# Performance work log

Measured on AMD Instinct MI355X. Metric: run time of the kernel, lower is better.

Reference implementation:

```python
import jax, jax.numpy as jnp
import numpy as np

B, S, D, H = 64, 512, 512, 512


def setup_inputs() -> dict:
    key = jax.random.key(0)
    ks = jax.random.split(key, 8)
    k = 1.0 / np.sqrt(H)  # torch nn.LSTM init bound
    return {
        "x": jax.random.normal(ks[0], (B, S, D), dtype=jnp.float32),
        "emb": jax.random.normal(ks[1], (B, D), dtype=jnp.float32),
        "h_n": jax.random.normal(ks[2], (1, B, H), dtype=jnp.float32),
        "c_n": jax.random.normal(ks[3], (1, B, H), dtype=jnp.float32),
        "W_ih": jax.random.uniform(ks[4], (4 * H, D), jnp.float32, -k, k),
        "W_hh": jax.random.uniform(ks[5], (4 * H, H), jnp.float32, -k, k),
        "b_ih": jax.random.uniform(ks[6], (4 * H,), jnp.float32, -k, k),
        "b_hh": jax.random.uniform(ks[7], (4 * H,), jnp.float32, -k, k),
    }


def reference(x, emb, h_n, c_n, W_ih, W_hh, b_ih, b_hh):
    # Decoder feeds emb at step 0, then teacher-forces x[:, i-1] at step i.
    inputs = jnp.concatenate([emb[:, None, :], x[:, :-1, :]], axis=1)  # [B,S,D]
    # Precompute input-to-hidden gates for the whole sequence (one big GEMM).
    xg = jnp.einsum("bsd,gd->bsg", inputs, W_ih) + b_ih + b_hh  # [B,S,4H]

    def step(carry, xg_t):
        h, c = carry
        gates = xg_t + h @ W_hh.T  # [B,4H]; torch gate order: i,f,g,o
        i, f, g, o = jnp.split(gates, 4, axis=-1)
        c = jax.nn.sigmoid(f) * c + jax.nn.sigmoid(i) * jnp.tanh(g)
        h = jax.nn.sigmoid(o) * jnp.tanh(c)
        return (h, c), h

    (_, _), ys = jax.lax.scan(step, (h_n[0], c_n[0]), jnp.swapaxes(xg, 0, 1))
    return jnp.swapaxes(ys, 0, 1)  # [B,S,H]
```

## Files before the change

### kernel.cpp

```cpp
#include <hip/hip_runtime.h>
#include <cstdint>


#define SS 512
#define DD 512
#define HH 512

typedef __attribute__((ext_vector_type(8))) short s8;
typedef __attribute__((ext_vector_type(4))) float f4;

__device__ inline short f2bf(float f) {
  unsigned u = __float_as_uint(f);
  u += 0x7fffu + ((u >> 16) & 1u);
  return (short)(u >> 16);
}

__device__ inline s8 cvt8(f4 a, f4 b) {
  s8 v;
  v[0]=f2bf(a[0]); v[1]=f2bf(a[1]); v[2]=f2bf(a[2]); v[3]=f2bf(a[3]);
  v[4]=f2bf(b[0]); v[5]=f2bf(b[1]); v[6]=f2bf(b[2]); v[7]=f2bf(b[3]);
  return v;
}

__device__ inline float sigm(float x)  { return 1.f / (1.f + __expf(-x)); }
__device__ inline float tanh_f(float x){ return 1.f - 2.f / (__expf(2.f*x) + 1.f); }

__device__ inline void stq_agent(void* p, unsigned long long v) {
  __hip_atomic_store((unsigned long long*)p, v, __ATOMIC_RELAXED, __HIP_MEMORY_SCOPE_AGENT);
}
__device__ inline unsigned long long ldq_agent(const void* p) {
  return __hip_atomic_load((const unsigned long long*)p, __ATOMIC_RELAXED, __HIP_MEMORY_SCOPE_AGENT);
}
__device__ inline void st4_agent(unsigned* p, unsigned v) {
  __hip_atomic_store(p, v, __ATOMIC_RELAXED, __HIP_MEMORY_SCOPE_AGENT);
}
__device__ inline unsigned ld4_agent(const unsigned* p) {
  return __hip_atomic_load(p, __ATOMIC_RELAXED, __HIP_MEMORY_SCOPE_AGENT);
}
__device__ inline void drain_vm() {
  asm volatile("s_waitcnt vmcnt(0)" ::: "memory");
}

__device__ inline void heavy_barrier(unsigned* cnt, unsigned target) {
  drain_vm();
  __syncthreads();
  if (threadIdx.x == 0) {
    __threadfence();
    __hip_atomic_fetch_add(cnt, 1u, __ATOMIC_RELAXED, __HIP_MEMORY_SCOPE_AGENT);
    unsigned guard = 0;
    while (__hip_atomic_load(cnt, __ATOMIC_RELAXED, __HIP_MEMORY_SCOPE_AGENT) < target) {
      __builtin_amdgcn_s_sleep(2);
      if (++guard > 10000000u) break;
    }
  }
  __syncthreads();
  (void)__hip_atomic_load(cnt, __ATOMIC_ACQUIRE, __HIP_MEMORY_SCOPE_AGENT);
  __syncthreads();
}

__launch_bounds__(256, 1)
__global__ void lstm_kernel(const float* __restrict__ x,   const float* __restrict__ emb,
                            const float* __restrict__ h_n, const float* __restrict__ c_n,
                            const float* __restrict__ W_ih, const float* __restrict__ W_hh,
                            const float* __restrict__ b_ih, const float* __restrict__ b_hh,
                            float* __restrict__ out, char* __restrict__ ws)
{
  const int tid  = threadIdx.x;
  const int wave = tid >> 6, lane = tid & 63;
  const int quad = lane >> 4, n = lane & 15;
  const int c  = blockIdx.x & 7;
  const int wg = blockIdx.x >> 3;

  unsigned* cnt   = (unsigned*)(ws + (size_t)c * 128);
  unsigned* flags = (unsigned*)(ws + 1024 + (size_t)c * 128);
  char*     hbuf  = ws + 4096;
  char*     xfrag = ws + 4096 + 2*8*8192;
  char*     xfc   = xfrag + (size_t)c * ((size_t)SS * 8192);

  __shared__ float lout[2][128];

  {
    int widc = wg*4 + wave;
    for (int item = widc; item < 4096; item += 128) {
      int t = item & 511, bl = item >> 9;
      const float* src = (t == 0) ? (emb + (size_t)(c*8 + bl) * DD)
                                  : (x + ((size_t)(c*8 + bl) * SS + (t-1)) * DD);
      f4 f0 = *(const f4*)(src + lane*8);
      f4 f1 = *(const f4*)(src + lane*8 + 4);
      s8 v = cvt8(f0, f1);
      *(s8*)(xfc + (size_t)t*8192 + (lane>>2)*512 + (lane&3)*128 + bl*16) = v;
    }
  }

  s8 wihf[16], whhf[16];
  {
    int r = wave*16 + n;
    int rowg = (r & 3)*512 + wg*16 + (r >> 2);
    const float* pih = W_ih + (size_t)rowg * DD + quad*8;
    const float* phh = W_hh + (size_t)rowg * HH + quad*8;
#pragma unroll
    for (int kk = 0; kk < 16; ++kk) {
      f4 a0 = *(const f4*)(pih + kk*32);
      f4 a1 = *(const f4*)(pih + kk*32 + 4);
      wihf[kk] = cvt8(a0, a1);
      f4 b0 = *(const f4*)(phh + kk*32);
      f4 b1 = *(const f4*)(phh + kk*32 + 4);
      whhf[kk] = cvt8(b0, b1);
    }
  }

  const int u = wg*16 + wave*4 + quad;
  f4 biasv;
  biasv[0] = b_ih[0*512+u] + b_hh[0*512+u];
  biasv[1] = b_ih[1*512+u] + b_hh[1*512+u];
  biasv[2] = b_ih[2*512+u] + b_hh[2*512+u];
  biasv[3] = b_ih[3*512+u] + b_hh[3*512+u];
  float creg = 0.f, h0 = 0.f;
  if (n < 8) {
    creg = c_n[(size_t)(c*8 + n)*HH + u];
    h0   = h_n[(size_t)(c*8 + n)*HH + u];
  }
  const int u0 = wg*16 + wave*4;
  const int hsoff = (u0>>5)*512 + ((u0>>3)&3)*128 + (u0&7)*2;

  {
    int sv = (int)(unsigned short)f2bf(h0);
    int p2 = sv | (__shfl_xor(sv, 16) << 16);
    int p4 = __shfl_xor(p2, 32);
    unsigned long long packed = (unsigned)p2 | ((unsigned long long)(unsigned)p4 << 32);
    if (lane < 8) stq_agent(hbuf + (size_t)c*8192 + hsoff + lane*16, packed);
  }

  heavy_barrier(cnt, 32u);

  const s8 zero8 = {0,0,0,0,0,0,0,0};
  s8 xf[16], hf[16];
#pragma unroll
  for (int kk = 0; kk < 16; ++kk) { xf[kk] = zero8; hf[kk] = zero8; }

  f4 accx = biasv, accx2 = {0.f,0.f,0.f,0.f};
  if (n < 8) {
    const char* xb = xfc + quad*128 + n*16;
#pragma unroll
    for (int kk = 0; kk < 16; ++kk)
      xf[kk] = *(const s8*)(xb + kk*512);
  }
#pragma unroll
  for (int kk = 0; kk < 8; ++kk)
    accx  = __builtin_amdgcn_mfma_f32_16x16x32_bf16(wihf[kk],   xf[kk],   accx,  0,0,0);
#pragma unroll
  for (int kk = 0; kk < 8; ++kk)
    accx2 = __builtin_amdgcn_mfma_f32_16x16x32_bf16(wihf[kk+8], xf[kk+8], accx2, 0,0,0);

  float* const outb = out + (size_t)(c*8)*SS*HH + wg*16;

  for (int t = 0; t < SS; ++t) {
    if (t > 0) {
      if (tid < 64) {
        const unsigned* fp = flags + (lane & 31);
        unsigned guard = 0; bool ok;
        do {
          ok = (ld4_agent(fp) >= (unsigned)t);
          if (++guard > 100000u) break;
        } while (!__all(ok));
      }
      __syncthreads();
    }

    const char* hrd = hbuf + (size_t)(((t  )&1)*8 + c)*8192;
    char*       hwr = hbuf + (size_t)(((t+1)&1)*8 + c)*8192;

    if (n < 8) {
      const char* b0 = hrd + quad*128 + n*16;
      union { unsigned long long qq[2]; s8 v; } tmp;
#pragma unroll
      for (int kk = 0; kk < 16; ++kk) {
        tmp.qq[0] = ldq_agent(b0 + kk*512);
        tmp.qq[1] = ldq_agent(b0 + kk*512 + 8);
        hf[kk] = tmp.v;
      }
    }

    f4 acc = accx, acc2 = accx2;
#pragma unroll
    for (int kk = 0; kk < 8; ++kk)
      acc  = __builtin_amdgcn_mfma_f32_16x16x32_bf16(whhf[kk],   hf[kk],   acc,  0,0,0);
#pragma unroll
    for (int kk = 0; kk < 8; ++kk)
      acc2 = __builtin_amdgcn_mfma_f32_16x16x32_bf16(whhf[kk+8], hf[kk+8], acc2, 0,0,0);
    acc += acc2;

    float iv = sigm(acc[0]);
    float fv = sigm(acc[1]);
    float gv = tanh_f(acc[2]);
    float ov = sigm(acc[3]);
    creg = fv*creg + iv*gv;
    float hv = ov * tanh_f(creg);

    if (n < 8) lout[t&1][n*16 + wave*4 + quad] = hv;

    if (t < SS-1) {
      int sv = (int)(unsigned short)f2bf(hv);
      int p2 = sv | (__shfl_xor(sv, 16) << 16);
      int p4 = __shfl_xor(p2, 32);
      unsigned long long packed = (unsigned)p2 | ((unsigned long long)(unsigned)p4 << 32);
      if (lane < 8) stq_agent(hwr + hsoff + lane*16, packed);
    }

    drain_vm();
    __syncthreads();

    if (t < SS-1 && tid == 0)
      st4_agent(flags + wg, (unsigned)(t + 1));

    if (tid < 128) {
      int n2 = tid >> 4, ul = tid & 15;
      outb[((size_t)n2*SS + t)*HH + ul] = lout[t&1][n2*16 + ul];
    }

    if (t < SS-1) {
      if (n < 8) {
        const char* xb = xfc + (size_t)(t+1)*8192 + quad*128 + n*16;
#pragma unroll
        for (int kk = 0; kk < 16; ++kk)
          xf[kk] = *(const s8*)(xb + kk*512);
      }
      accx = biasv; accx2[0]=0.f; accx2[1]=0.f; accx2[2]=0.f; accx2[3]=0.f;
#pragma unroll
      for (int kk = 0; kk < 8; ++kk)
        accx  = __builtin_amdgcn_mfma_f32_16x16x32_bf16(wihf[kk],   xf[kk],   accx,  0,0,0);
#pragma unroll
      for (int kk = 0; kk < 8; ++kk)
        accx2 = __builtin_amdgcn_mfma_f32_16x16x32_bf16(wihf[kk+8], xf[kk+8], accx2, 0,0,0);
    }
  }
}

extern "C" void kernel_launch(void* const* d_in, const int* in_sizes, int n_in,
                              void* d_out, int out_size, void* d_ws, size_t ws_size,
                              hipStream_t stream) {
  const float* x    = (const float*)d_in[0];
  const float* emb  = (const float*)d_in[1];
  const float* h_n  = (const float*)d_in[2];
  const float* c_n  = (const float*)d_in[3];
  const float* W_ih = (const float*)d_in[4];
  const float* W_hh = (const float*)d_in[5];
  const float* b_ih = (const float*)d_in[6];
  const float* b_hh = (const float*)d_in[7];

  hipMemsetAsync(d_ws, 0, 2048, stream);

  lstm_kernel<<<dim3(256), dim3(256), 0, stream>>>(
      x, emb, h_n, c_n, W_ih, W_hh, b_ih, b_hh, (float*)d_out, (char*)d_ws);
}
```

Before: 1.672 ms.

## Replace block-wide step barrier with per-wave flag counters and partial h prefetch

```diff
diff --git a/kernel.cpp b/kernel.cpp
--- a/kernel.cpp
+++ b/kernel.cpp
@@ -31,14 +31,17 @@
 __device__ inline unsigned long long ldq_agent(const void* p) {
   return __hip_atomic_load((const unsigned long long*)p, __ATOMIC_RELAXED, __HIP_MEMORY_SCOPE_AGENT);
 }
-__device__ inline void st4_agent(unsigned* p, unsigned v) {
-  __hip_atomic_store(p, v, __ATOMIC_RELAXED, __HIP_MEMORY_SCOPE_AGENT);
-}
 __device__ inline unsigned ld4_agent(const unsigned* p) {
   return __hip_atomic_load(p, __ATOMIC_RELAXED, __HIP_MEMORY_SCOPE_AGENT);
 }
 __device__ inline void drain_vm() {
   asm volatile("s_waitcnt vmcnt(0)" ::: "memory");
+}
+
+__device__ inline unsigned flag_ballot(const unsigned* flags, int lane, unsigned target) {
+  unsigned v = ld4_agent(flags + (lane & 31));
+  unsigned long long b = __ballot(v >= target);
+  return (unsigned)b & (unsigned)(b >> 32);
 }
 
 __device__ inline void heavy_barrier(unsigned* cnt, unsigned target) {
@@ -85,8 +88,8 @@
       int t = item & 511, bl = item >> 9;
       const float* src = (t == 0) ? (emb + (size_t)(c*8 + bl) * DD)
                                   : (x + ((size_t)(c*8 + bl) * SS + (t-1)) * DD);
-      f4 f0 = *(const f4*)(src + lane*8);
-      f4 f1 = *(const f4*)(src + lane*8 + 4);
+      f4 f0 = __builtin_nontemporal_load((const f4*)(src + lane*8));
+      f4 f1 = __builtin_nontemporal_load((const f4*)(src + lane*8 + 4));
       s8 v = cvt8(f0, f1);
       *(s8*)(xfc + (size_t)t*8192 + (lane>>2)*512 + (lane&3)*128 + bl*16) = v;
     }
@@ -143,7 +146,7 @@
     const char* xb = xfc + quad*128 + n*16;
 #pragma unroll
     for (int kk = 0; kk < 16; ++kk)
-      xf[kk] = *(const s8*)(xb + kk*512);
+      xf[kk] = __builtin_nontemporal_load((const s8*)(xb + kk*512));
   }
 #pragma unroll
   for (int kk = 0; kk < 8; ++kk)
@@ -152,32 +155,45 @@
   for (int kk = 0; kk < 8; ++kk)
     accx2 = __builtin_amdgcn_mfma_f32_16x16x32_bf16(wihf[kk+8], xf[kk+8], accx2, 0,0,0);
 
+  unsigned pm = 0xFFFFu;
+  unsigned rdy = 0u;
+  if (n < 8) {
+    const char* b0 = hbuf + (size_t)c*8192 + quad*128 + n*16;
+#pragma unroll
+    for (int kk = 0; kk < 16; ++kk) {
+      union { unsigned long long qq[2]; s8 v; } tmp;
+      tmp.qq[0] = ldq_agent(b0 + kk*512);
+      tmp.qq[1] = ldq_agent(b0 + kk*512 + 8);
+      hf[kk] = tmp.v;
+    }
+  }
+
   float* const outb = out + (size_t)(c*8)*SS*HH + wg*16;
 
   for (int t = 0; t < SS; ++t) {
-    if (t > 0) {
-      if (tid < 64) {
-        const unsigned* fp = flags + (lane & 31);
-        unsigned guard = 0; bool ok;
-        do {
-          ok = (ld4_agent(fp) >= (unsigned)t);
-          if (++guard > 100000u) break;
-        } while (!__all(ok));
-      }
-      __syncthreads();
-    }
-
     const char* hrd = hbuf + (size_t)(((t  )&1)*8 + c)*8192;
     char*       hwr = hbuf + (size_t)(((t+1)&1)*8 + c)*8192;
-
-    if (n < 8) {
-      const char* b0 = hrd + quad*128 + n*16;
-      union { unsigned long long qq[2]; s8 v; } tmp;
+    const unsigned tgt = 4u * (unsigned)t;
+
+    if (pm != 0xFFFFu) {
 #pragma unroll
       for (int kk = 0; kk < 16; ++kk) {
-        tmp.qq[0] = ldq_agent(b0 + kk*512);
-        tmp.qq[1] = ldq_agent(b0 + kk*512 + 8);
-        hf[kk] = tmp.v;
+        if (!(pm & (1u << kk))) {
+          const unsigned need = 3u << (2*kk);
+          unsigned guard = 0;
+          while ((rdy & need) != need) {
+            rdy |= flag_ballot(flags, lane, tgt);
+            asm volatile("" ::: "memory");
+            if (++guard > 1000000u) break;
+          }
+          if (n < 8) {
+            const char* b0 = hrd + quad*128 + n*16;
+            union { unsigned long long qq[2]; s8 v; } tmp;
+            tmp.qq[0] = ldq_agent(b0 + kk*512);
+            tmp.qq[1] = ldq_agent(b0 + kk*512 + 8);
+            hf[kk] = tmp.v;
+          }
+        }
       }
     }
 
@@ -205,17 +221,24 @@
       int p4 = __shfl_xor(p2, 32);
       unsigned long long packed = (unsigned)p2 | ((unsigned long long)(unsigned)p4 << 32);
       if (lane < 8) stq_agent(hwr + hsoff + lane*16, packed);
-    }
-
-    drain_vm();
+      drain_vm();
+      if (lane == 0)
+        __hip_atomic_fetch_add(flags + wg, 1u, __ATOMIC_RELAXED, __HIP_MEMORY_SCOPE_AGENT);
+    }
+
+    const unsigned tgt1 = 4u * (unsigned)(t+1);
+    pm = 0u; rdy = 0u;
+    if (t < SS-1) {
+      rdy = flag_ballot(flags, lane, tgt1);
+      asm volatile("" ::: "memory");
+    }
+
     __syncthreads();
-
-    if (t < SS-1 && tid == 0)
-      st4_agent(flags + wg, (unsigned)(t + 1));
 
     if (tid < 128) {
       int n2 = tid >> 4, ul = tid & 15;
-      outb[((size_t)n2*SS + t)*HH + ul] = lout[t&1][n2*16 + ul];
+      __builtin_nontemporal_store(lout[t&1][n2*16 + ul],
+                                  &outb[((size_t)n2*SS + t)*HH + ul]);
     }
 
     if (t < SS-1) {
@@ -223,7 +246,7 @@
         const char* xb = xfc + (size_t)(t+1)*8192 + quad*128 + n*16;
 #pragma unroll
         for (int kk = 0; kk < 16; ++kk)
-          xf[kk] = *(const s8*)(xb + kk*512);
+          xf[kk] = __builtin_nontemporal_load((const s8*)(xb + kk*512));
       }
       accx = biasv; accx2[0]=0.f; accx2[1]=0.f; accx2[2]=0.f; accx2[3]=0.f;
 #pragma unroll
@@ -232,6 +255,23 @@
 #pragma unroll
       for (int kk = 0; kk < 8; ++kk)
         accx2 = __builtin_amdgcn_mfma_f32_16x16x32_bf16(wihf[kk+8], xf[kk+8], accx2, 0,0,0);
+
+      rdy |= flag_ballot(flags, lane, tgt1);
+      asm volatile("" ::: "memory");
+#pragma unroll
+      for (int kk = 0; kk < 16; ++kk) {
+        const unsigned need = 3u << (2*kk);
+        if ((rdy & need) == need) {
+          if (n < 8) {
+            const char* b1 = hwr + quad*128 + n*16;
+            union { unsigned long long qq[2]; s8 v; } tmp;
+            tmp.qq[0] = ldq_agent(b1 + kk*512);
+            tmp.qq[1] = ldq_agent(b1 + kk*512 + 8);
+            hf[kk] = tmp.v;
+          }
+          pm |= 1u << kk;
+        }
+      }
     }
   }
 }
```

After: 4.961 ms. 197% more time.
